# Optimization experiments

Hardware: AMD Instinct MI355X
Metric: run time of the kernel (lower is better)

Reference implementation:

```python
import jax, jax.numpy as jnp
import numpy as np
from functools import partial

B, H, W = 2, 480, 480
C, HALF = 32, 16
L, WN, PAD = 4, 20, 20

def gelu(x):
    return jax.nn.gelu(x, approximate=False)

def setup_inputs() -> dict:
    key = jax.random.key(0)
    ks = jax.random.split(key, 24)
    scale = 1.0 / (C * C)
    d = {}
    d["input_data"] = jax.random.normal(ks[0], (B, H, W, 1), jnp.float32)
    d["src_data"] = jax.random.normal(ks[1], (B, H, W, 3), jnp.float32)
    # input lifting MLP: sizes [5, 16, 32]
    d["in_w1"] = jax.random.normal(ks[2], (5, HALF), jnp.float32) * 0.1
    d["in_b1"] = jnp.zeros((HALF,), jnp.float32)
    d["in_w2"] = jax.random.normal(ks[3], (HALF, C), jnp.float32) * 0.1
    d["in_b2"] = jnp.zeros((C,), jnp.float32)
    # eps lifting MLP: sizes [3, 16, 32]
    d["eps_w1"] = jax.random.normal(ks[4], (3, HALF), jnp.float32) * 0.1
    d["eps_b1"] = jnp.zeros((HALF,), jnp.float32)
    d["eps_w2"] = jax.random.normal(ks[5], (HALF, C), jnp.float32) * 0.1
    d["eps_b2"] = jnp.zeros((C,), jnp.float32)
    # Fourier layer params, stacked over L layers
    d["fw1"] = jax.random.uniform(ks[6], (L, C, C, WN, WN, 2), jnp.float32) * scale
    d["fw2"] = jax.random.uniform(ks[7], (L, C, C, WN, WN, 2), jnp.float32) * scale
    d["conv_w"] = jax.random.normal(ks[8], (L, C, C), jnp.float32) * 0.05
    d["conv_b"] = jnp.zeros((L, C), jnp.float32)
    # projection MLP: sizes [32, 16, 2]
    d["proj_w1"] = jax.random.normal(ks[9], (C, HALF), jnp.float32) * 0.1
    d["proj_b1"] = jnp.zeros((HALF,), jnp.float32)
    d["proj_w2"] = jax.random.normal(ks[10], (HALF, 2), jnp.float32) * 0.1
    d["proj_b2"] = jnp.zeros((2,), jnp.float32)
    # mask conv 3x3, 1->1 channel
    d["mask_w"] = jax.random.normal(ks[11], (1, 1, 3, 3), jnp.float32) * 0.1
    d["mask_b"] = jnp.zeros((1,), jnp.float32)
    return d

def _grid(b, h, w):
    gx = jnp.broadcast_to(jnp.linspace(0.0, 1.0, h, dtype=jnp.float32)[None, :, None, None], (b, h, w, 1))
    gy = jnp.broadcast_to(jnp.linspace(0.0, 1.0, w, dtype=jnp.float32)[None, None, :, None], (b, h, w, 1))
    return jnp.concatenate([gx, gy], axis=-1)

def _mlp(x, w1, b1, w2, b2):
    # FCLayer(gelu) then FCLayer(linear)
    return gelu(x @ w1 + b1) @ w2 + b2

def _fourier_conv(x, x_eps, w1, w2):
    # x, x_eps: [B, C, Hp, Wp]
    hp, wp = x.shape[-2], x.shape[-1]
    xf = jnp.fft.rfft2(x * x_eps)                       # [B,C,Hp,Wp//2+1] complex
    xr = jnp.stack([xf.real, xf.imag], axis=-1)         # [B,C,Hp,Wp//2+1,2]
    lo = jnp.einsum('bixyz,ioxyz->boxyz', xr[:, :, :WN, :WN, :], w1)
    hi = jnp.einsum('bixyz,ioxyz->boxyz', xr[:, :, -WN:, :WN, :], w2)
    out = jnp.zeros((x.shape[0], w1.shape[1], hp, wp // 2 + 1, 2), jnp.float32)
    out = out.at[:, :, :WN, :WN, :].set(lo)
    out = out.at[:, :, -WN:, :WN, :].set(hi)
    return jnp.fft.irfft2(out[..., 0] + 1j * out[..., 1], s=(hp, wp))

def _forward(input_data, src_data, in_w1, in_b1, in_w2, in_b2,
             eps_w1, eps_b1, eps_w2, eps_b2, fw1, fw2, conv_w, conv_b,
             proj_w1, proj_b1, proj_w2, proj_b2, mask_w, mask_b):
    b, h, w = input_data.shape[0], input_data.shape[1], input_data.shape[2]
    grid = _grid(b, h, w)
    x_in = jnp.concatenate([src_data, grid], axis=-1)       # [B,H,W,5]
    x_eps = jnp.concatenate([input_data, grid], axis=-1)    # [B,H,W,3]
    field = src_data[..., 1:]                               # [B,H,W,2]

    a = _mlp(x_in, in_w1, in_b1, in_w2, in_b2)              # [B,H,W,C]
    a = jnp.transpose(a, (0, 3, 1, 2))                      # [B,C,H,W]
    a = jnp.pad(a, ((0, 0), (0, 0), (0, PAD), (0, PAD)))    # [B,C,H+P,W+P]
    e = _mlp(x_eps, eps_w1, eps_b1, eps_w2, eps_b2)
    e = jnp.transpose(e, (0, 3, 1, 2))
    e = jnp.pad(e, ((0, 0), (0, 0), (0, PAD), (0, PAD)))

    for l in range(L):
        x1 = _fourier_conv(a, e, fw1[l], fw2[l])
        x2 = jnp.einsum('bihw,oi->bohw', a, conv_w[l]) + conv_b[l][None, :, None, None]
        a = x1 + x2
        if l < L - 1:
            a = gelu(a)

    pred = a[..., :-PAD, :-PAD]                             # [B,C,H,W]
    pred = jnp.transpose(pred, (0, 2, 3, 1))                # [B,H,W,C]
    pred = _mlp(pred, proj_w1, proj_b1, proj_w2, proj_b2)   # [B,H,W,2]

    xm = jnp.transpose(input_data, (0, 3, 1, 2))            # [B,1,H,W]
    mask = jax.lax.conv_general_dilated(xm, mask_w, (1, 1), 'SAME',
                                        dimension_numbers=('NCHW', 'OIHW', 'NCHW'))
    mask = mask + mask_b[None, :, None, None]
    mask = jnp.transpose(mask, (0, 2, 3, 1))                # [B,H,W,1] -> broadcasts over 2
    return field * mask + pred

def reference(input_data, src_data, in_w1, in_b1, in_w2, in_b2,
              eps_w1, eps_b1, eps_w2, eps_b2, fw1, fw2, conv_w, conv_b,
              proj_w1, proj_b1, proj_w2, proj_b2, mask_w, mask_b):
    return _forward(input_data, src_data, in_w1, in_b1, in_w2, in_b2,
                    eps_w1, eps_b1, eps_w2, eps_b2, fw1, fw2, conv_w, conv_b,
                    proj_w1, proj_b1, proj_w2, proj_b2, mask_w, mask_b)
```

## Files before the change

kernel.cpp:

```cpp
#include <hip/hip_runtime.h>
#include <hip/hip_bf16.h>

#define BD 2
#define HD 480
#define WD 480
#define CD 32
#define HALFD 16
#define WND 20
#define NP 500
#define PLANE (HD*WD)
#define TWO_PI_OVER_NP 0.012566370614359172954f

typedef __attribute__((ext_vector_type(8))) short bf16x8;
typedef __attribute__((ext_vector_type(4))) float f32x4;

__device__ __forceinline__ float gelu_f(float x) {
    return 0.5f * x * (1.0f + erff(x * 0.70710678118654752f));
}
__device__ __forceinline__ float bfbits2f(short s) {
    unsigned u = ((unsigned)(unsigned short)s) << 16;
    return __uint_as_float(u);
}
__device__ __forceinline__ short bf16s(float v) {
    __hip_bfloat16 b = __float2bfloat16(v);
    return *reinterpret_cast<short*>(&b);
}
__device__ __forceinline__ unsigned pk2(float a, float b) {
    return (unsigned)(unsigned short)bf16s(a) | ((unsigned)(unsigned short)bf16s(b) << 16);
}

__global__ void __launch_bounds__(256) k_ae(
    const float* src, const float* inp,
    const float* iw1, const float* ib1,
    const float* iw2, const float* ib2,
    const float* ew1, const float* eb1,
    const float* ew2, const float* eb2,
    __hip_bfloat16* A, __hip_bfloat16* E)
{
    __shared__ float s_iw1[80], s_ib1[16];
    __shared__ float s_ew1[48], s_eb1[16];
    __shared__ __align__(16) __hip_bfloat16 s_hidA[256 * 24];
    __shared__ __align__(16) __hip_bfloat16 s_hidE[256 * 24];
    __shared__ __align__(16) __hip_bfloat16 s_out[32 * 264];

    int tid = threadIdx.x;
    int lane = tid & 63, wv = tid >> 6;

    if (tid < 80) s_iw1[tid] = iw1[tid];
    if (tid >= 96 && tid < 112) s_ib1[tid - 96] = ib1[tid - 96];
    if (tid >= 128 && tid < 176) s_ew1[tid - 128] = ew1[tid - 128];
    if (tid >= 192 && tid < 208) s_eb1[tid - 192] = eb1[tid - 192];

    int c0 = lane & 15, kg = lane >> 4;
    bf16x8 bIn[2], bEps[2];
    float biasIn[2], biasEps[2];
    #pragma unroll
    for (int nt = 0; nt < 2; nt++) {
        int c = nt * 16 + c0;
        #pragma unroll
        for (int j = 0; j < 8; j++) {
            int k = kg * 8 + j;
            bIn[nt][j]  = (k < 16) ? bf16s(iw2[k * 32 + c]) : (short)0;
            bEps[nt][j] = (k < 16) ? bf16s(ew2[k * 32 + c]) : (short)0;
        }
        biasIn[nt]  = ib2[c];
        biasEps[nt] = eb2[c];
    }
    __syncthreads();

    int gid = blockIdx.x * 256 + tid;
    int b = gid / PLANE;
    int r = gid % PLANE;
    int h = r / WD, w = r % WD;
    float gx = (float)h * (1.0f / 479.0f);
    float gy = (float)w * (1.0f / 479.0f);
    float s0 = src[(size_t)gid * 3 + 0];
    float s1 = src[(size_t)gid * 3 + 1];
    float s2 = src[(size_t)gid * 3 + 2];
    float xi = inp[gid];

    {
        unsigned pk[8];
        #pragma unroll
        for (int j = 0; j < 16; j += 2) {
            float v0 = s_ib1[j]     + s0 * s_iw1[j]     + s1 * s_iw1[16 + j]
                     + s2 * s_iw1[32 + j]     + gx * s_iw1[48 + j]     + gy * s_iw1[64 + j];
            float v1 = s_ib1[j + 1] + s0 * s_iw1[j + 1] + s1 * s_iw1[16 + j + 1]
                     + s2 * s_iw1[32 + j + 1] + gx * s_iw1[48 + j + 1] + gy * s_iw1[64 + j + 1];
            pk[j >> 1] = pk2(gelu_f(v0), gelu_f(v1));
        }
        uint4* d = reinterpret_cast<uint4*>(&s_hidA[tid * 24]);
        d[0] = make_uint4(pk[0], pk[1], pk[2], pk[3]);
        d[1] = make_uint4(pk[4], pk[5], pk[6], pk[7]);
        #pragma unroll
        for (int j = 0; j < 16; j += 2) {
            float v0 = s_eb1[j]     + xi * s_ew1[j]     + gx * s_ew1[16 + j]     + gy * s_ew1[32 + j];
            float v1 = s_eb1[j + 1] + xi * s_ew1[j + 1] + gx * s_ew1[16 + j + 1] + gy * s_ew1[32 + j + 1];
            pk[j >> 1] = pk2(gelu_f(v0), gelu_f(v1));
        }
        uint4* d2 = reinterpret_cast<uint4*>(&s_hidE[tid * 24]);
        d2[0] = make_uint4(pk[0], pk[1], pk[2], pk[3]);
        d2[1] = make_uint4(pk[4], pk[5], pk[6], pk[7]);
    }
    __syncthreads();

    int r0 = (blockIdx.x % 900) * 256;

    #pragma unroll
    for (int pass = 0; pass < 2; pass++) {
        const __hip_bfloat16* hid = pass ? s_hidE : s_hidA;
        #pragma unroll
        for (int t = 0; t < 4; t++) {
            int tile = wv * 4 + t;
            bf16x8 av = {0, 0, 0, 0, 0, 0, 0, 0};
            if (kg < 2)
                av = *reinterpret_cast<const bf16x8*>(&hid[(tile * 16 + c0) * 24 + kg * 8]);
            #pragma unroll
            for (int nt = 0; nt < 2; nt++) {
                f32x4 acc = {0.f, 0.f, 0.f, 0.f};
                bf16x8 bv = pass ? bEps[nt] : bIn[nt];
                acc = __builtin_amdgcn_mfma_f32_16x16x32_bf16(av, bv, acc, 0, 0, 0);
                float bias = pass ? biasEps[nt] : biasIn[nt];
                int ch = nt * 16 + c0;
                int px = tile * 16 + kg * 4;
                unsigned w0 = pk2(acc[0] + bias, acc[1] + bias);
                unsigned w1 = pk2(acc[2] + bias, acc[3] + bias);
                *reinterpret_cast<uint2*>(&s_out[ch * 264 + px]) = make_uint2(w0, w1);
            }
        }
        __syncthreads();
        __hip_bfloat16* dst = (pass ? E : A) + (size_t)b * CD * PLANE + r0;
        #pragma unroll
        for (int i = 0; i < 4; i++) {
            int idx = tid + i * 256;
            int ch = idx >> 5, chunk = idx & 31;
            uint4 v = *reinterpret_cast<const uint4*>(&s_out[ch * 264 + chunk * 8]);
            *reinterpret_cast<uint4*>(&dst[(size_t)ch * PLANE + chunk * 8]) = v;
        }
        __syncthreads();
    }
}

__global__ void k_tables(__hip_bfloat16* T) {
    int e = blockIdx.x * 256 + threadIdx.x;
    if (e >= 435 * 512) return;
    int tile = e >> 9, r = e & 511;
    int lane = r >> 3, j = r & 7;
    float v = 0.0f;
    if (tile < 45) {
        int kt = tile / 3, nt = tile % 3;
        int k = kt * 32 + ((lane >> 4) << 3) + j;
        int n = nt * 16 + (lane & 15);
        if (n < 40) {
            int ky = n >> 1;
            int idx = (k * ky) % NP;
            float ang = (float)idx * TWO_PI_OVER_NP;
            v = (n & 1) ? -sinf(ang) : cosf(ang);
        }
    } else if (tile < 105) {
        int t2 = tile - 45;
        int nt = t2 >> 1, kt = t2 & 1;
        int kk = kt * 32 + ((lane >> 4) << 3) + j;
        int w = nt * 16 + (lane & 15);
        if (kk < 40) {
            int ky = kk >> 1;
            int idx = (ky * w) % NP;
            float ang = (float)idx * TWO_PI_OVER_NP;
            v = (kk & 1) ? -sinf(ang) : cosf(ang);
        }
    } else if (tile < 255) {
        int t2 = tile - 105;
        int kt = t2 / 5, nt = t2 % 5;
        int k = kt * 32 + ((lane >> 4) << 3) + j;
        int n = nt * 16 + (lane & 15);
        int hh = k >> 1, ri = k & 1;
        int kxi = n >> 1, part = n & 1;
        int kx = (kxi < 20) ? kxi : kxi + 460;
        int idx = (kx * hh) % NP;
        float ang = (float)idx * TWO_PI_OVER_NP;
        float c = cosf(ang), s = sinf(ang);
        v = (part == 0) ? (ri == 0 ? c : s) : (ri == 0 ? -s : c);
    } else {
        int t2 = tile - 255;
        int nt = t2 / 3, kt = t2 % 3;
        int k = kt * 32 + ((lane >> 4) << 3) + j;
        int n = nt * 16 + (lane & 15);
        if (k < 80) {
            int kxi = k >> 1, ri = k & 1;
            int hh = n >> 1, part = n & 1;
            int kx = (kxi < 20) ? kxi : kxi + 460;
            int idx = (kx * hh) % NP;
            float ang = (float)idx * TWO_PI_OVER_NP;
            float c = cosf(ang), s = sinf(ang);
            v = (part == 0) ? (ri == 0 ? c : -s) : (ri == 0 ? s : c);
        }
    }
    T[e] = __float2bfloat16(v);
}

__global__ void __launch_bounds__(256) k_F1m(
    const __hip_bfloat16* A, const __hip_bfloat16* E,
    const __hip_bfloat16* Twig, __hip_bfloat16* Y1)
{
    int wv = threadIdx.x >> 6, lane = threadIdx.x & 63;
    int task = blockIdx.x * 4 + wv;
    int bh = task / 6, rem = task % 6;
    int mt = rem & 1, nt = rem >> 1;
    int b = bh / HD, h = bh % HD;
    int c = mt * 16 + (lane & 15);
    int koff = (lane >> 4) << 3;
    size_t base = ((size_t)(b * 32 + c)) * PLANE + (size_t)h * WD + koff;
    const __hip_bfloat16* arow = A + base;
    const __hip_bfloat16* erow = E + base;
    f32x4 acc = {0.f, 0.f, 0.f, 0.f};
    #pragma unroll
    for (int kt = 0; kt < 15; kt++) {
        bf16x8 av = *reinterpret_cast<const bf16x8*>(arow + kt * 32);
        bf16x8 ev = *reinterpret_cast<const bf16x8*>(erow + kt * 32);
        bf16x8 gv;
        #pragma unroll
        for (int j = 0; j < 8; j++)
            gv[j] = bf16s(bfbits2f(av[j]) * bfbits2f(ev[j]));
        bf16x8 bv = *reinterpret_cast<const bf16x8*>(Twig + (((kt * 3 + nt) << 9) + lane * 8));
        acc = __builtin_amdgcn_mfma_f32_16x16x32_bf16(gv, bv, acc, 0, 0, 0);
    }
    int n = nt * 16 + (lane & 15);
    if (n < 40) {
        int ky = n >> 1, part = n & 1;
        int crow = mt * 16 + ((lane >> 4) << 2);
        #pragma unroll
        for (int r = 0; r < 4; r++) {
            int cc = crow + r;
            Y1[((((size_t)(b * 32 + cc)) * WND + ky) * HD + h) * 2 + part] =
                __float2bfloat16(acc[r]);
        }
    }
}

__global__ void __launch_bounds__(256) k_F2m(
    const __hip_bfloat16* Y1, const __hip_bfloat16* Tf2, float* Y2)
{
    int wv = threadIdx.x >> 6, lane = threadIdx.x & 63;
    int task = blockIdx.x * 4 + wv;
    int mt = task / 5, nt = task % 5;
    int row = mt * 16 + (lane & 15);
    int koff = (lane >> 4) << 3;
    const __hip_bfloat16* arow = Y1 + (size_t)row * 960 + koff;
    f32x4 acc = {0.f, 0.f, 0.f, 0.f};
    #pragma unroll
    for (int kt = 0; kt < 30; kt++) {
        bf16x8 av = *reinterpret_cast<const bf16x8*>(arow + kt * 32);
        bf16x8 bv = *reinterpret_cast<const bf16x8*>(Tf2 + (((kt * 5 + nt) << 9) + lane * 8));
        acc = __builtin_amdgcn_mfma_f32_16x16x32_bf16(av, bv, acc, 0, 0, 0);
    }
    int n = nt * 16 + (lane & 15);
    int mb = mt * 16 + ((lane >> 4) << 2);
    #pragma unroll
    for (int r = 0; r < 4; r++)
        Y2[(size_t)(mb + r) * 80 + n] = acc[r];
}

__global__ void __launch_bounds__(256) k_mix(
    const float* Y2, __hip_bfloat16* Zb,
    const float* fw1, const float* fw2, int l)
{
    int gid = blockIdx.x * 256 + threadIdx.x;
    int col = gid % 96;
    int row = gid / 96;
    if (col >= 80) { Zb[gid] = __float2bfloat16(0.0f); return; }
    int ky = row % 20;
    int oc = (row / 20) % 32;
    int b = row / 640;
    int z = col & 1;
    int kxi = col >> 1;
    const float* wp;
    int x;
    if (kxi < 20) { wp = fw1; x = kxi; } else { wp = fw2; x = kxi - 20; }
    size_t wbase = ((((size_t)(l * 32) * 32 + oc) * 20 + x) * 20 + ky) * 2 + z;
    const float* y2 = Y2 + ((size_t)b * 32 * 20 + ky) * 80 + kxi * 2 + z;
    float acc = 0.f;
    for (int i = 0; i < 32; i++) {
        float yv = y2[(size_t)i * 1600];
        float wv = wp[wbase + (size_t)i * 25600];
        acc += yv * wv;
    }
    Zb[gid] = __float2bfloat16(acc);
}

__global__ void __launch_bounds__(256) k_I1m(
    const __hip_bfloat16* Zb, const __hip_bfloat16* Ti1, __hip_bfloat16* U)
{
    int wv = threadIdx.x >> 6, lane = threadIdx.x & 63;
    int task = blockIdx.x * 4 + wv;
    int mt = task / 60, nt = task % 60;
    int row = mt * 16 + (lane & 15);
    int koff = (lane >> 4) << 3;
    const __hip_bfloat16* arow = Zb + (size_t)row * 96 + koff;
    f32x4 acc = {0.f, 0.f, 0.f, 0.f};
    #pragma unroll
    for (int kt = 0; kt < 3; kt++) {
        bf16x8 av = *reinterpret_cast<const bf16x8*>(arow + kt * 32);
        bf16x8 bv = *reinterpret_cast<const bf16x8*>(Ti1 + (((nt * 3 + kt) << 9) + lane * 8));
        acc = __builtin_amdgcn_mfma_f32_16x16x32_bf16(av, bv, acc, 0, 0, 0);
    }
    int n = nt * 16 + (lane & 15);
    int mb = mt * 16 + ((lane >> 4) << 2);
    #pragma unroll
    for (int r = 0; r < 4; r++)
        U[(size_t)(mb + r) * 960 + n] = __float2bfloat16(acc[r]);
}

__global__ void __launch_bounds__(512) k_I2F1(
    const __hip_bfloat16* U, __hip_bfloat16* A,
    const __hip_bfloat16* E,
    const float* convw, const float* convb,
    const __hip_bfloat16* TinvF, const __hip_bfloat16* Twig,
    __hip_bfloat16* Y1, int l)
{
    __shared__ __align__(16) __hip_bfloat16 sUf[4 * 512];
    __shared__ __align__(16) __hip_bfloat16 sWf[2 * 512];
    __shared__ __align__(16) __hip_bfloat16 sA[32 * 488];
    __shared__ float sB[CD];
    int tid = threadIdx.x;
    int b = blockIdx.x / HD;
    int h = blockIdx.x % HD;
    if (tid < CD) sB[tid] = convb[l * CD + tid];
    for (int t = tid; t < 2048; t += 512) {
        int j = t & 7, lane = (t >> 3) & 63, ktmt = t >> 9;
        int mt = ktmt >> 1, kt = ktmt & 1;
        int oc = mt * 16 + (lane & 15);
        int kk = kt * 32 + ((lane >> 4) << 3) + j;
        float v = 0.f;
        if (kk < 40) {
            int ky = kk >> 1;
            __hip_bfloat162 u = reinterpret_cast<const __hip_bfloat162*>(U)
                [(((size_t)b * CD + oc) * WND + ky) * HD + h];
            float sc = (ky == 0 ? 1.0f : 2.0f) * (1.0f / 250000.0f);
            v = ((kk & 1) ? __bfloat162float(u.y) : __bfloat162float(u.x)) * sc;
        }
        sUf[t] = __float2bfloat16(v);
    }
    for (int t = tid; t < 1024; t += 512) {
        int j = t & 7, lane = (t >> 3) & 63, mt = t >> 9;
        int oc = mt * 16 + (lane & 15);
        int ic = ((lane >> 4) << 3) + j;
        sWf[t] = __float2bfloat16(convw[(size_t)l * CD * CD + oc * CD + ic]);
    }
    __syncthreads();
    int wv = tid >> 6, lane = tid & 63;
    int c0 = lane & 15, kg = lane >> 4;
    const unsigned short* Ap = reinterpret_cast<const unsigned short*>(A)
        + (size_t)b * CD * PLANE + (size_t)h * WD;
    for (int t = wv; t < 60; t += 8) {
        int mt = t & 1, nt = t >> 1;
        f32x4 acc = {0.f, 0.f, 0.f, 0.f};
        #pragma unroll
        for (int kt = 0; kt < 2; kt++) {
            bf16x8 av = *reinterpret_cast<const bf16x8*>(&sUf[((mt * 2 + kt) << 9) + lane * 8]);
            bf16x8 bv = *reinterpret_cast<const bf16x8*>(TinvF + (((nt * 2 + kt) << 9) + lane * 8));
            acc = __builtin_amdgcn_mfma_f32_16x16x32_bf16(av, bv, acc, 0, 0, 0);
        }
        bf16x8 av2 = *reinterpret_cast<const bf16x8*>(&sWf[(mt << 9) + lane * 8]);
        bf16x8 bv2;
        #pragma unroll
        for (int j = 0; j < 8; j++)
            bv2[j] = (short)Ap[(size_t)(kg * 8 + j) * PLANE + nt * 16 + c0];
        acc = __builtin_amdgcn_mfma_f32_16x16x32_bf16(av2, bv2, acc, 0, 0, 0);
        int w = nt * 16 + c0;
        int ocb = mt * 16 + (kg << 2);
        #pragma unroll
        for (int r = 0; r < 4; r++) {
            short sv = bf16s(gelu_f(acc[r] + sB[ocb + r]));
            sA[(ocb + r) * 488 + w] = *reinterpret_cast<__hip_bfloat16*>(&sv);
        }
    }
    __syncthreads();
    {
        __hip_bfloat16* Adst = A + (size_t)b * CD * PLANE + (size_t)h * WD;
        for (int t = tid; t < 32 * 60; t += 512) {
            int row = t / 60, chunk = t % 60;
            uint4 v = *reinterpret_cast<const uint4*>(&sA[row * 488 + chunk * 8]);
            *reinterpret_cast<uint4*>(&Adst[(size_t)row * PLANE + chunk * 8]) = v;
        }
    }
    for (int t = wv; t < 6; t += 8) {
        int mt = t & 1, nt = t >> 1;
        int c = mt * 16 + c0;
        const __hip_bfloat16* erow =
            E + ((size_t)(b * 32 + c)) * PLANE + (size_t)h * WD + (kg << 3);
        const __hip_bfloat16* albase = &sA[c * 488 + (kg << 3)];
        f32x4 acc = {0.f, 0.f, 0.f, 0.f};
        #pragma unroll
        for (int kt = 0; kt < 15; kt++) {
            bf16x8 av = *reinterpret_cast<const bf16x8*>(albase + kt * 32);
            bf16x8 ev = *reinterpret_cast<const bf16x8*>(erow + kt * 32);
            bf16x8 gv;
            #pragma unroll
            for (int j = 0; j < 8; j++)
                gv[j] = bf16s(bfbits2f(av[j]) * bfbits2f(ev[j]));
            bf16x8 bv = *reinterpret_cast<const bf16x8*>(Twig + (((kt * 3 + nt) << 9) + lane * 8));
            acc = __builtin_amdgcn_mfma_f32_16x16x32_bf16(gv, bv, acc, 0, 0, 0);
        }
        int n = nt * 16 + c0;
        if (n < 40) {
            int ky = n >> 1, part = n & 1;
            int crow = mt * 16 + (kg << 2);
            #pragma unroll
            for (int r = 0; r < 4; r++) {
                int cc = crow + r;
                Y1[((((size_t)(b * 32 + cc)) * WND + ky) * HD + h) * 2 + part] =
                    __float2bfloat16(acc[r]);
            }
        }
    }
}

__global__ void __launch_bounds__(512) k_I2out(
    const __hip_bfloat16* U, const __hip_bfloat16* A,
    const float* convw, const float* convb,
    const __hip_bfloat16* TinvF,
    const float* inp, const float* src,
    const float* pw1, const float* pb1,
    const float* pw2, const float* pb2,
    const float* mw, const float* mb,
    float* out, int l)
{
    __shared__ __align__(16) __hip_bfloat16 sUf[4 * 512];
    __shared__ __align__(16) __hip_bfloat16 sWf[2 * 512];
    __shared__ __hip_bfloat16 sAT[WD * 33];
    __shared__ float sB[CD];
    __shared__ float sW1[CD * HALFD], sB1[HALFD], sW2[HALFD * 2], sB2[2], sM[9], sMB[1];
    int tid = threadIdx.x;
    int b = blockIdx.x / HD;
    int h = blockIdx.x % HD;
    if (tid < CD) sB[tid] = convb[l * CD + tid];
    sW1[tid] = pw1[tid];
    if (tid >= 32 && tid < 48) sB1[tid - 32] = pb1[tid - 32];
    if (tid >= 64 && tid < 96) sW2[tid - 64] = pw2[tid - 64];
    if (tid >= 96 && tid < 98) sB2[tid - 96] = pb2[tid - 96];
    if (tid >= 128 && tid < 137) sM[tid - 128] = mw[tid - 128];
    if (tid == 160) sMB[0] = mb[0];
    for (int t = tid; t < 2048; t += 512) {
        int j = t & 7, lane = (t >> 3) & 63, ktmt = t >> 9;
        int mt = ktmt >> 1, kt = ktmt & 1;
        int oc = mt * 16 + (lane & 15);
        int kk = kt * 32 + ((lane >> 4) << 3) + j;
        float v = 0.f;
        if (kk < 40) {
            int ky = kk >> 1;
            __hip_bfloat162 u = reinterpret_cast<const __hip_bfloat162*>(U)
                [(((size_t)b * CD + oc) * WND + ky) * HD + h];
            float sc = (ky == 0 ? 1.0f : 2.0f) * (1.0f / 250000.0f);
            v = ((kk & 1) ? __bfloat162float(u.y) : __bfloat162float(u.x)) * sc;
        }
        sUf[t] = __float2bfloat16(v);
    }
    for (int t = tid; t < 1024; t += 512) {
        int j = t & 7, lane = (t >> 3) & 63, mt = t >> 9;
        int oc = mt * 16 + (lane & 15);
        int ic = ((lane >> 4) << 3) + j;
        sWf[t] = __float2bfloat16(convw[(size_t)l * CD * CD + oc * CD + ic]);
    }
    __syncthreads();
    int wv = tid >> 6, lane = tid & 63;
    int c0 = lane & 15, kg = lane >> 4;
    const unsigned short* Ap = reinterpret_cast<const unsigned short*>(A)
        + (size_t)b * CD * PLANE + (size_t)h * WD;
    for (int t = wv; t < 60; t += 8) {
        int mt = t & 1, nt = t >> 1;
        f32x4 acc = {0.f, 0.f, 0.f, 0.f};
        #pragma unroll
        for (int kt = 0; kt < 2; kt++) {
            bf16x8 av = *reinterpret_cast<const bf16x8*>(&sUf[((mt * 2 + kt) << 9) + lane * 8]);
            bf16x8 bv = *reinterpret_cast<const bf16x8*>(TinvF + (((nt * 2 + kt) << 9) + lane * 8));
            acc = __builtin_amdgcn_mfma_f32_16x16x32_bf16(av, bv, acc, 0, 0, 0);
        }
        bf16x8 av2 = *reinterpret_cast<const bf16x8*>(&sWf[(mt << 9) + lane * 8]);
        bf16x8 bv2;
        #pragma unroll
        for (int j = 0; j < 8; j++)
            bv2[j] = (short)Ap[(size_t)(kg * 8 + j) * PLANE + nt * 16 + c0];
        acc = __builtin_amdgcn_mfma_f32_16x16x32_bf16(av2, bv2, acc, 0, 0, 0);
        int w = nt * 16 + c0;
        int ocb = mt * 16 + (kg << 2);
        #pragma unroll
        for (int r = 0; r < 4; r++) {
            short sv = bf16s(acc[r] + sB[ocb + r]);
            sAT[w * 33 + (ocb + r)] = *reinterpret_cast<__hip_bfloat16*>(&sv);
        }
    }
    __syncthreads();
    for (int w = tid; w < WD; w += 512) {
        float av[32];
        #pragma unroll
        for (int i = 0; i < 32; i++) av[i] = bfbits2f(
            *reinterpret_cast<const short*>(&sAT[w * 33 + i]));
        float hid[16];
        #pragma unroll
        for (int j = 0; j < 16; j++) {
            float v = sB1[j];
            #pragma unroll
            for (int i = 0; i < 32; i++) v += av[i] * sW1[i * 16 + j];
            hid[j] = gelu_f(v);
        }
        float p0 = sB2[0], p1 = sB2[1];
        #pragma unroll
        for (int j = 0; j < 16; j++) { p0 += hid[j] * sW2[j * 2]; p1 += hid[j] * sW2[j * 2 + 1]; }
        float m = sMB[0];
        #pragma unroll
        for (int dh = 0; dh < 3; dh++) {
            int hh = h + dh - 1;
            #pragma unroll
            for (int dw = 0; dw < 3; dw++) {
                int ww = w + dw - 1;
                if (hh >= 0 && hh < HD && ww >= 0 && ww < WD)
                    m += inp[(size_t)b * PLANE + (size_t)hh * WD + ww] * sM[dh * 3 + dw];
            }
        }
        size_t gid = (size_t)b * PLANE + (size_t)h * WD + w;
        float f0 = src[gid * 3 + 1];
        float f1 = src[gid * 3 + 2];
        out[gid * 2 + 0] = f0 * m + p0;
        out[gid * 2 + 1] = f1 * m + p1;
    }
}

extern "C" void kernel_launch(void* const* d_in, const int* in_sizes, int n_in,
                              void* d_out, int out_size, void* d_ws, size_t ws_size,
                              hipStream_t stream) {
    const float* inp = (const float*)d_in[0];
    const float* src = (const float*)d_in[1];
    const float* iw1 = (const float*)d_in[2];
    const float* ib1 = (const float*)d_in[3];
    const float* iw2 = (const float*)d_in[4];
    const float* ib2 = (const float*)d_in[5];
    const float* ew1 = (const float*)d_in[6];
    const float* eb1 = (const float*)d_in[7];
    const float* ew2 = (const float*)d_in[8];
    const float* eb2 = (const float*)d_in[9];
    const float* fw1 = (const float*)d_in[10];
    const float* fw2 = (const float*)d_in[11];
    const float* cw  = (const float*)d_in[12];
    const float* cb  = (const float*)d_in[13];
    const float* pw1 = (const float*)d_in[14];
    const float* pb1 = (const float*)d_in[15];
    const float* pw2 = (const float*)d_in[16];
    const float* pb2 = (const float*)d_in[17];
    const float* mw  = (const float*)d_in[18];
    const float* mb  = (const float*)d_in[19];

    const size_t NA = (size_t)BD * CD * PLANE;
    __hip_bfloat16* A   = (__hip_bfloat16*)d_ws;
    __hip_bfloat16* E   = A + NA;
    __hip_bfloat16* Y1U = E + NA;
    float* Y2 = (float*)(Y1U + (size_t)BD * CD * WND * HD * 2);
    __hip_bfloat16* Zb = (__hip_bfloat16*)(Y2 + 1280 * 80);
    __hip_bfloat16* Tbl   = Zb + 1280 * 96;
    __hip_bfloat16* Twig  = Tbl;
    __hip_bfloat16* TinvF = Twig + 45 * 512;
    __hip_bfloat16* Tf2   = TinvF + 60 * 512;
    __hip_bfloat16* Ti1   = Tf2 + 150 * 512;

    k_tables<<<870, 256, 0, stream>>>(Tbl);
    k_ae<<<1800, 256, 0, stream>>>(src, inp, iw1, ib1, iw2, ib2,
                                   ew1, eb1, ew2, eb2, A, E);

    k_F1m<<<1440, 256, 0, stream>>>(A, E, Twig, Y1U);
    for (int l = 0; l < 4; l++) {
        k_F2m<<<100, 256, 0, stream>>>(Y1U, Tf2, Y2);
        k_mix<<<480, 256, 0, stream>>>(Y2, Zb, fw1, fw2, l);
        k_I1m<<<1200, 256, 0, stream>>>(Zb, Ti1, Y1U);
        if (l < 3)
            k_I2F1<<<BD * HD, 512, 0, stream>>>(Y1U, A, E, cw, cb, TinvF, Twig,
                                                Y1U, l);
        else
            k_I2out<<<BD * HD, 512, 0, stream>>>(Y1U, A, cw, cb, TinvF,
                                                 inp, src, pw1, pb1, pw2, pb2,
                                                 mw, mb, (float*)d_out, l);
    }
}
```

Baseline: 394.8 us.

## Fuse second forward DFT, spectral mixing and first inverse DFT into one kernel

Replaces three per-layer launches (F2 GEMM, spectral channel mixing, I1 GEMM) with one kernel per (batch, ky) block that keeps the Y2 and Zb intermediates in shared memory. This removes two kernel launches and the global round trips of small intermediates per layer. In exchange the fused kernel has only 40 blocks of 1024 threads, so far fewer CUs are busy and phases serialize within a block. Only 10 of 16 waves do work in the first GEMM phase. In-place reads and writes of Y1U are safe because each block touches only its own ky rows.

```diff
diff --git a/kernel.cpp b/kernel.cpp
--- a/kernel.cpp
+++ b/kernel.cpp
@@ -237,77 +237,74 @@
     }
 }
 
-__global__ void __launch_bounds__(256) k_F2m(
-    const __hip_bfloat16* Y1, const __hip_bfloat16* Tf2, float* Y2)
-{
-    int wv = threadIdx.x >> 6, lane = threadIdx.x & 63;
-    int task = blockIdx.x * 4 + wv;
-    int mt = task / 5, nt = task % 5;
-    int row = mt * 16 + (lane & 15);
-    int koff = (lane >> 4) << 3;
-    const __hip_bfloat16* arow = Y1 + (size_t)row * 960 + koff;
-    f32x4 acc = {0.f, 0.f, 0.f, 0.f};
-    #pragma unroll
-    for (int kt = 0; kt < 30; kt++) {
-        bf16x8 av = *reinterpret_cast<const bf16x8*>(arow + kt * 32);
-        bf16x8 bv = *reinterpret_cast<const bf16x8*>(Tf2 + (((kt * 5 + nt) << 9) + lane * 8));
-        acc = __builtin_amdgcn_mfma_f32_16x16x32_bf16(av, bv, acc, 0, 0, 0);
-    }
-    int n = nt * 16 + (lane & 15);
-    int mb = mt * 16 + ((lane >> 4) << 2);
-    #pragma unroll
-    for (int r = 0; r < 4; r++)
-        Y2[(size_t)(mb + r) * 80 + n] = acc[r];
-}
-
-__global__ void __launch_bounds__(256) k_mix(
-    const float* Y2, __hip_bfloat16* Zb,
+__global__ void __launch_bounds__(1024) k_FMI(
+    __hip_bfloat16* Y1U, const __hip_bfloat16* Tf2, const __hip_bfloat16* Ti1,
     const float* fw1, const float* fw2, int l)
 {
-    int gid = blockIdx.x * 256 + threadIdx.x;
-    int col = gid % 96;
-    int row = gid / 96;
-    if (col >= 80) { Zb[gid] = __float2bfloat16(0.0f); return; }
-    int ky = row % 20;
-    int oc = (row / 20) % 32;
-    int b = row / 640;
-    int z = col & 1;
-    int kxi = col >> 1;
-    const float* wp;
-    int x;
-    if (kxi < 20) { wp = fw1; x = kxi; } else { wp = fw2; x = kxi - 20; }
-    size_t wbase = ((((size_t)(l * 32) * 32 + oc) * 20 + x) * 20 + ky) * 2 + z;
-    const float* y2 = Y2 + ((size_t)b * 32 * 20 + ky) * 80 + kxi * 2 + z;
-    float acc = 0.f;
-    for (int i = 0; i < 32; i++) {
-        float yv = y2[(size_t)i * 1600];
-        float wv = wp[wbase + (size_t)i * 25600];
-        acc += yv * wv;
-    }
-    Zb[gid] = __float2bfloat16(acc);
-}
-
-__global__ void __launch_bounds__(256) k_I1m(
-    const __hip_bfloat16* Zb, const __hip_bfloat16* Ti1, __hip_bfloat16* U)
-{
-    int wv = threadIdx.x >> 6, lane = threadIdx.x & 63;
-    int task = blockIdx.x * 4 + wv;
-    int mt = task / 60, nt = task % 60;
-    int row = mt * 16 + (lane & 15);
-    int koff = (lane >> 4) << 3;
-    const __hip_bfloat16* arow = Zb + (size_t)row * 96 + koff;
-    f32x4 acc = {0.f, 0.f, 0.f, 0.f};
-    #pragma unroll
-    for (int kt = 0; kt < 3; kt++) {
-        bf16x8 av = *reinterpret_cast<const bf16x8*>(arow + kt * 32);
-        bf16x8 bv = *reinterpret_cast<const bf16x8*>(Ti1 + (((nt * 3 + kt) << 9) + lane * 8));
-        acc = __builtin_amdgcn_mfma_f32_16x16x32_bf16(av, bv, acc, 0, 0, 0);
-    }
-    int n = nt * 16 + (lane & 15);
-    int mb = mt * 16 + ((lane >> 4) << 2);
-    #pragma unroll
-    for (int r = 0; r < 4; r++)
-        U[(size_t)(mb + r) * 960 + n] = __float2bfloat16(acc[r]);
+    __shared__ float sY2[32 * 80];
+    __shared__ __align__(16) __hip_bfloat16 sZb[32 * 104];
+    int tid = threadIdx.x;
+    int lane = tid & 63, wv = tid >> 6;
+    int c0 = lane & 15, kg = lane >> 4;
+    int koff = kg * 8;
+    int b = blockIdx.x / WND;
+    int ky = blockIdx.x % WND;
+
+    for (int t = wv; t < 10; t += 16) {
+        int mt = t % 2, nt = t / 2;
+        const __hip_bfloat16* arow = Y1U
+            + ((size_t)(b * 32 + mt * 16 + c0) * WND + ky) * 960 + koff;
+        f32x4 acc = {0.f, 0.f, 0.f, 0.f};
+        #pragma unroll
+        for (int kt = 0; kt < 30; kt++) {
+            bf16x8 av = *reinterpret_cast<const bf16x8*>(arow + kt * 32);
+            bf16x8 bv = *reinterpret_cast<const bf16x8*>(Tf2 + (((kt * 5 + nt) << 9) + lane * 8));
+            acc = __builtin_amdgcn_mfma_f32_16x16x32_bf16(av, bv, acc, 0, 0, 0);
+        }
+        int col = nt * 16 + c0;
+        int mb = mt * 16 + kg * 4;
+        #pragma unroll
+        for (int r = 0; r < 4; r++)
+            sY2[(mb + r) * 80 + col] = acc[r];
+    }
+    __syncthreads();
+
+    for (int o = tid; o < 2560; o += 1024) {
+        int oc = o / 80, col = o % 80;
+        int z = col & 1, kxi = col >> 1;
+        const float* wp;
+        int x;
+        if (kxi < 20) { wp = fw1; x = kxi; } else { wp = fw2; x = kxi - 20; }
+        size_t wbase = ((((size_t)(l * 32) * 32 + oc) * 20 + x) * 20 + ky) * 2 + z;
+        float acc = 0.f;
+        #pragma unroll 8
+        for (int i = 0; i < 32; i++)
+            acc += sY2[i * 80 + col] * wp[wbase + (size_t)i * 25600];
+        sZb[oc * 104 + col] = __float2bfloat16(acc);
+    }
+    if (tid < 512) {
+        int oc = tid >> 4, cp = 80 + (tid & 15);
+        sZb[oc * 104 + cp] = __float2bfloat16(0.0f);
+    }
+    __syncthreads();
+
+    for (int t = wv; t < 120; t += 16) {
+        int mt = t / 60, nt = t % 60;
+        const __hip_bfloat16* azb = &sZb[(mt * 16 + c0) * 104 + koff];
+        f32x4 acc = {0.f, 0.f, 0.f, 0.f};
+        #pragma unroll
+        for (int kt = 0; kt < 3; kt++) {
+            bf16x8 av = *reinterpret_cast<const bf16x8*>(azb + kt * 32);
+            bf16x8 bv = *reinterpret_cast<const bf16x8*>(Ti1 + (((nt * 3 + kt) << 9) + lane * 8));
+            acc = __builtin_amdgcn_mfma_f32_16x16x32_bf16(av, bv, acc, 0, 0, 0);
+        }
+        int n = nt * 16 + c0;
+        int mb = mt * 16 + kg * 4;
+        #pragma unroll
+        for (int r = 0; r < 4; r++)
+            Y1U[((size_t)(b * 32 + mb + r) * WND + ky) * 960 + n] =
+                __float2bfloat16(acc[r]);
+    }
 }
 
 __global__ void __launch_bounds__(512) k_I2F1(
@@ -567,9 +564,7 @@
 
     k_F1m<<<1440, 256, 0, stream>>>(A, E, Twig, Y1U);
     for (int l = 0; l < 4; l++) {
-        k_F2m<<<100, 256, 0, stream>>>(Y1U, Tf2, Y2);
-        k_mix<<<480, 256, 0, stream>>>(Y2, Zb, fw1, fw2, l);
-        k_I1m<<<1200, 256, 0, stream>>>(Zb, Ti1, Y1U);
+        k_FMI<<<BD * WND, 1024, 0, stream>>>(Y1U, Tf2, Ti1, fw1, fw2, l);
         if (l < 3)
             k_I2F1<<<BD * HD, 512, 0, stream>>>(Y1U, A, E, cw, cb, TinvF, Twig,
                                                 Y1U, l);
```

Result: slower. 561.9 us (+42.3%).
